# Performance work log

Measured on AMD Instinct MI355X. Metric: run time of the kernel, lower is better.

## Reference

```python
import jax, jax.numpy as jnp
import numpy as np

B, A, D, H, F = 256, 96, 384, 192, 96   # molecules, atoms, feat, hidden, species-MLP out
S = 4                                   # number of species (H, C, N, O)
E = B * A * 32                          # edges (avg degree 32)
CUTOFF = 5.2


def smooth_cutoff(d, cutoff):
    # Smoothstep-style cutoff: 1 at d=0, smoothly -> 0 at d=cutoff (Smoothstep class, reversed edges)
    x = jnp.clip((cutoff - d) / cutoff, 0.0, 1.0)
    return x ** 3 * (x * (6.0 * x - 15.0) + 10.0)


def setup_inputs() -> dict:
    key = jax.random.key(0)
    ks = jax.random.split(key, 9)
    species = jax.random.randint(ks[0], (B, A), 0, S, dtype=jnp.int32)
    in_features = jax.random.normal(ks[1], (B, A, D), dtype=jnp.float32)
    atom_index12 = jax.random.randint(ks[2], (2, E), 0, B * A, dtype=jnp.int32)
    distances = jax.random.uniform(ks[3], (E,), jnp.float32, 0.1, CUTOFF)
    total_charges = jnp.zeros((B,), jnp.float32)
    W1 = jax.random.normal(ks[4], (S, D, H), jnp.float32) / np.float32(np.sqrt(D))
    W2 = jax.random.normal(ks[5], (S, H, F), jnp.float32) / np.float32(np.sqrt(H))
    Wn = jax.random.normal(ks[6], (S, F, F), jnp.float32) / np.float32(np.sqrt(F))
    Wf = jax.random.normal(ks[7], (S, 2 * F, 1), jnp.float32) / np.float32(np.sqrt(2 * F))
    return dict(species=species, in_features=in_features, atom_index12=atom_index12,
                distances=distances, total_charges=total_charges,
                W1=W1, W2=W2, Wn=Wn, Wf=Wf,
                decay_prefactor=jnp.asarray(1.0, jnp.float32),
                decay_factor=jnp.asarray(1.0, jnp.float32))


def reference(species, in_features, atom_index12, distances, total_charges,
              W1, W2, Wn, Wf, decay_prefactor, decay_factor):
    b, a, d = in_features.shape
    n = b * a
    sp = species.reshape(-1)                      # [N]
    x = in_features.reshape(n, d)                 # [N, D]

    # per-species main MLP dispatch: internal[i] = MLP_{sp[i]}(x[i])
    internal = jnp.zeros((n, F), x.dtype)
    for s in range(S):
        mask = (sp == s)[:, None]
        h = jax.nn.gelu(x @ W1[s]) @ W2[s]        # [N, F]
        internal = internal + jnp.where(mask, h, jnp.zeros((), x.dtype))

    # per-species neighbor MLP
    nbr = jnp.zeros((n, F), x.dtype)
    for s in range(S):
        mask = (sp == s)[:, None]
        nbr = nbr + jnp.where(mask, internal @ Wn[s], jnp.zeros((), x.dtype))

    # distance-decayed edge messages: merged[i0] += nbr[i1]*w, merged[i1] += nbr[i0]*w
    decay = (decay_prefactor ** 2) * jnp.exp(-(decay_factor ** 2) * distances) \
            * smooth_cutoff(distances, CUTOFF)    # [E]
    i0, i1 = atom_index12[0], atom_index12[1]
    m_to_i0 = nbr[i1] * decay[:, None]            # [E, F]
    m_to_i1 = nbr[i0] * decay[:, None]
    merged = jax.ops.segment_sum(jnp.concatenate([m_to_i0, m_to_i1], axis=0),
                                 jnp.concatenate([i0, i1], axis=0),
                                 num_segments=n)  # [N, F]

    feats = jnp.concatenate([internal, merged], axis=-1)  # [N, 2F]

    # per-species final head -> precharges
    precharges = jnp.zeros((n,), x.dtype)
    for s in range(S):
        mask = (sp == s)
        precharges = precharges + jnp.where(mask, (feats @ Wf[s])[:, 0], jnp.zeros((), x.dtype))
    precharges = precharges.reshape(b, a)

    # total-charge redistribution (uniform factors, no learned redistribution)
    dummy_mask = species != -1
    factors = 1.0 / dummy_mask.sum(-1, keepdims=True).astype(x.dtype)
    charges = precharges + (total_charges - precharges.sum(-1))[:, None] * factors
    charges = jnp.where(dummy_mask, charges, jnp.zeros((), x.dtype))
    return species, charges, precharges
```

## Files before the change

### kernel.cpp

```cpp
#include <hip/hip_runtime.h>
#include <cstdint>
#include <cstddef>

#define NBm 256
#define NAm 96
#define NDm 384
#define NHm 192
#define NFm 96
#define NSm 4
#define NATOMS (NBm*NAm)
#define NEe (NATOMS*32)
#define CUTOFF_ 5.2f
#define PBLK 256
#define EPB (NEe/PBLK)
#define HBLK 96

typedef __attribute__((ext_vector_type(8))) short short8;
typedef __attribute__((ext_vector_type(4))) float float4v;

__device__ __forceinline__ short f2bf(float f){
  union { float f; unsigned u; } v; v.f = f;
  unsigned r = v.u + 0x7FFFu + ((v.u >> 16) & 1u);
  return (short)(r >> 16);
}

__device__ __forceinline__ float gelu_t(float x){
  float u = 0.7978845608028654f * (x + 0.044715f * x*x*x);
  float e = __expf(-2.0f * fabsf(u));
  float t = (1.0f - e) / (1.0f + e);
  t = (u >= 0.f) ? t : -t;
  return 0.5f * x * (1.0f + t);
}

#define W1N (NSm*NDm*NHm)
#define W2N (NSm*NHm*NFm)
#define WNN (NSm*NFm*NFm)
#define WTOT (W1N+W2N+WNN)
#define WBLK (WTOT/256)
__global__ __launch_bounds__(256) void k_prep(
    const float* __restrict__ W1, const float* __restrict__ W2,
    const float* __restrict__ Wn, const int* __restrict__ sp,
    short* __restrict__ W1t, short* __restrict__ W2t, short* __restrict__ Wnt,
    int* __restrict__ Pcnt){
  int b = blockIdx.x;
  if (b < WBLK){
    int idx = b*256 + threadIdx.x;
    if (idx < W1N){
      int s = idx / (NDm*NHm); int rem = idx - s*NDm*NHm;
      int k = rem / NHm, c = rem - k*NHm;
      W1t[(s*NHm + c)*NDm + k] = f2bf(W1[idx]);
    } else if (idx < W1N + W2N){
      int j = idx - W1N;
      int s = j / (NHm*NFm); int rem = j - s*NHm*NFm;
      int k = rem / NFm, c = rem - k*NFm;
      W2t[(s*NFm + c)*NHm + k] = f2bf(W2[j]);
    } else {
      int j = idx - W1N - W2N;
      int s = j / (NFm*NFm); int rem = j - s*NFm*NFm;
      int k = rem / NFm, c = rem - k*NFm;
      Wnt[(s*NFm + c)*NFm + k] = f2bf(Wn[j]);
    }
  } else {
    __shared__ int h[NSm];
    int t = threadIdx.x;
    if (t < NSm) h[t] = 0;
    __syncthreads();
    int i = (b - WBLK)*256 + t;
    atomicAdd(&h[sp[i]], 1);
    __syncthreads();
    if (t < NSm) Pcnt[(b - WBLK)*NSm + t] = h[t];
  }
}

__global__ __launch_bounds__(256) void k_order(const int* __restrict__ sp,
    const int* __restrict__ Pcnt, int* __restrict__ sps, int* __restrict__ order){
  __shared__ int P[HBLK][NSm];
  __shared__ int stot[NSm], spre[NSm], sscan[NSm+1];
  __shared__ int base[NSm], h[NSm];
  int t = threadIdx.x, b = blockIdx.x;
  if (t < HBLK){
    #pragma unroll
    for (int j=0;j<NSm;j++) P[t][j] = Pcnt[t*NSm + j];
  }
  if (t < NSm) h[t] = 0;
  __syncthreads();
  if (t < NSm){
    int tot = 0, pr = 0;
    for (int bb=0; bb<HBLK; bb++){
      if (bb == b) pr = tot;
      tot += P[bb][t];
    }
    stot[t] = tot; spre[t] = pr;
  }
  __syncthreads();
  if (t == 0){
    int r = 0;
    #pragma unroll
    for (int s2=0;s2<NSm;s2++){ sscan[s2] = r; r += stot[s2]; }
    sscan[NSm] = r;
    if (b == 0){
      #pragma unroll
      for (int s2=0;s2<=NSm;s2++) sps[s2] = sscan[s2];
    }
  }
  __syncthreads();
  if (t < NSm) base[t] = sscan[t] + spre[t];
  __syncthreads();
  int i = b*256 + t;
  int s = sp[i];
  int lr = atomicAdd(&h[s], 1);
  order[base[s] + lr] = i;
}

__global__ __launch_bounds__(256) void k_mlp(
    const float* __restrict__ X, const int* __restrict__ order,
    const int* __restrict__ sps,
    const short* __restrict__ W1t, const short* __restrict__ W2t,
    const short* __restrict__ Wnt, const float* __restrict__ Wf,
    float* __restrict__ pre, float* __restrict__ nd4){
  const int s = blockIdx.y;
  const int s0 = sps[s];
  const int cnt = sps[s+1] - s0;
  const int row0 = blockIdx.x * 64;
  if (row0 >= cnt) return;

  __shared__ short Hs[64][200];
  __shared__ short Is[64][104];
  __shared__ short Ws[19968];
  __shared__ int aids[64];

  const int tid = threadIdx.x;
  if (tid < 64){
    int r = row0 + tid;
    aids[tid] = order[s0 + ((r < cnt) ? r : 0)];
  }
  __syncthreads();

  const int wave = tid >> 6, lane = tid & 63;
  const int lrow = lane & 15, quad = lane >> 4;
  const int arow = wave*16 + lrow;
  const float* xrow = X + (size_t)aids[arow]*NDm + quad*8;

  short8 afs[12];
  #pragma unroll
  for (int kb=0; kb<12; kb++){
    const float* p = xrow + kb*32;
    #pragma unroll
    for (int j=0;j<8;j++) afs[kb][j] = f2bf(p[j]);
  }

  const short* W1s = W1t + (size_t)s*NHm*NDm;
  float4v acc[12];
  #pragma unroll
  for (int i=0;i<12;i++){ acc[i][0]=0.f; acc[i][1]=0.f; acc[i][2]=0.f; acc[i][3]=0.f; }
  for (int kc=0; kc<4; kc++){
    __syncthreads();
    for (int e = tid; e < 192*12; e += 256){
      int c = e / 12, u = e - c*12;
      *(short8*)(&Ws[c*104 + u*8]) = *(const short8*)(W1s + c*NDm + kc*96 + u*8);
    }
    __syncthreads();
    #pragma unroll
    for (int kb3=0; kb3<3; kb3++){
      short8 af = afs[kc*3 + kb3];
      #pragma unroll
      for (int ct=0; ct<12; ct++){
        short8 bfb = *(const short8*)(&Ws[(ct*16 + lrow)*104 + kb3*32 + quad*8]);
        acc[ct] = __builtin_amdgcn_mfma_f32_16x16x32_bf16(af, bfb, acc[ct], 0,0,0);
      }
    }
  }
  #pragma unroll
  for (int ct=0; ct<12; ct++){
    #pragma unroll
    for (int r=0;r<4;r++){
      Hs[wave*16 + quad*4 + r][ct*16 + lrow] = f2bf(gelu_t(acc[ct][r]));
    }
  }

  const short* W2s = W2t + (size_t)s*NFm*NHm;
  float4v acc2[6];
  #pragma unroll
  for (int i=0;i<6;i++){ acc2[i][0]=0.f; acc2[i][1]=0.f; acc2[i][2]=0.f; acc2[i][3]=0.f; }
  __syncthreads();
  for (int e = tid; e < 96*24; e += 256){
    int c = e / 24, u = e - c*24;
    *(short8*)(&Ws[c*200 + u*8]) = *(const short8*)(W2s + c*NHm + u*8);
  }
  __syncthreads();
  for (int kb=0; kb<6; kb++){
    short8 af2 = *(const short8*)(&Hs[wave*16 + lrow][kb*32 + quad*8]);
    #pragma unroll
    for (int ct=0; ct<6; ct++){
      short8 bfb = *(const short8*)(&Ws[(ct*16 + lrow)*200 + kb*32 + quad*8]);
      acc2[ct] = __builtin_amdgcn_mfma_f32_16x16x32_bf16(af2, bfb, acc2[ct], 0,0,0);
    }
  }
  #pragma unroll
  for (int ct=0; ct<6; ct++){
    #pragma unroll
    for (int r=0;r<4;r++){
      Is[wave*16 + quad*4 + r][ct*16 + lrow] = f2bf(acc2[ct][r]);
    }
  }

  {
    float pr[4] = {0.f,0.f,0.f,0.f};
    #pragma unroll
    for (int ct=0; ct<6; ct++){
      float wv = Wf[s*2*NFm + ct*16 + lrow];
      #pragma unroll
      for (int r=0;r<4;r++) pr[r] += acc2[ct][r] * wv;
    }
    #pragma unroll
    for (int m=1; m<16; m<<=1){
      #pragma unroll
      for (int r=0;r<4;r++) pr[r] += __shfl_xor(pr[r], m, 64);
    }
    if (lrow == 0){
      #pragma unroll
      for (int r=0;r<4;r++){
        int row = wave*16 + quad*4 + r;
        if (row0 + row < cnt) pre[aids[row]] = pr[r];
      }
    }
  }

  const short* Wns = Wnt + (size_t)s*NFm*NFm;
  float4v acc3[6];
  #pragma unroll
  for (int i=0;i<6;i++){ acc3[i][0]=0.f; acc3[i][1]=0.f; acc3[i][2]=0.f; acc3[i][3]=0.f; }
  __syncthreads();
  for (int e = tid; e < 96*12; e += 256){
    int c = e / 12, u = e - c*12;
    *(short8*)(&Ws[c*104 + u*8]) = *(const short8*)(Wns + c*NFm + u*8);
  }
  __syncthreads();
  for (int kb=0; kb<3; kb++){
    short8 af3 = *(const short8*)(&Is[wave*16 + lrow][kb*32 + quad*8]);
    #pragma unroll
    for (int ct=0; ct<6; ct++){
      short8 bfb = *(const short8*)(&Ws[(ct*16 + lrow)*104 + kb*32 + quad*8]);
      acc3[ct] = __builtin_amdgcn_mfma_f32_16x16x32_bf16(af3, bfb, acc3[ct], 0,0,0);
    }
  }

  {
    float* NL = (float*)Ws;
    __syncthreads();
    #pragma unroll
    for (int ct=0; ct<6; ct++){
      #pragma unroll
      for (int r=0;r<4;r++){
        NL[(wave*16 + quad*4 + r)*97 + ct*16 + lrow] = acc3[ct][r];
      }
    }
    __syncthreads();
    int row = tid >> 2, t2 = tid & 3;
    if (row0 + row < cnt){
      const float* wfp = Wf + t2*2*NFm + NFm;
      const float* nlr = NL + row*97;
      float a4 = 0.f;
      #pragma unroll 8
      for (int j=0;j<NFm;j++) a4 += nlr[j] * wfp[j];
      nd4[(size_t)aids[row]*4 + t2] = a4;
    }
  }
}

__global__ __launch_bounds__(1024) void k_eacc(const int* __restrict__ ai,
    const float* __restrict__ dist, const float* __restrict__ pref,
    const float* __restrict__ fac, const int* __restrict__ sp,
    const float* __restrict__ nd4, float* __restrict__ part){
  __shared__ float acc[NATOMS];
  const int t = threadIdx.x, b = blockIdx.x;
  #pragma unroll
  for (int k=0;k<NATOMS/1024;k++) acc[k*1024 + t] = 0.f;
  __syncthreads();
  const float p = pref[0], fc = fac[0];
  const int base = b*EPB;
  #pragma unroll
  for (int k=0;k<EPB/1024;k++){
    int e = base + k*1024 + t;
    int i0 = ai[e];
    int i1 = ai[NEe + e];
    float d = dist[e];
    int s0 = sp[i0], s1 = sp[i1];
    float4v n1v = *(const float4v*)(nd4 + (size_t)i1*4);
    float4v n0v = *(const float4v*)(nd4 + (size_t)i0*4);
    float x = (CUTOFF_ - d) * (1.0f/CUTOFF_);
    x = fminf(fmaxf(x, 0.f), 1.f);
    float sc = x*x*x*(x*(6.f*x - 15.f) + 10.f);
    float w = p*p * expf(-fc*fc*d) * sc;
    float a1 = (s0 < 2) ? ((s0 == 0) ? n1v[0] : n1v[1]) : ((s0 == 2) ? n1v[2] : n1v[3]);
    float a0 = (s1 < 2) ? ((s1 == 0) ? n0v[0] : n0v[1]) : ((s1 == 2) ? n0v[2] : n0v[3]);
    atomicAdd(&acc[i0], w * a1);
    atomicAdd(&acc[i1], w * a0);
  }
  __syncthreads();
  float* dst = part + (size_t)b*NATOMS;
  for (int k=t; k<NATOMS/4; k+=1024){
    *(float4v*)(dst + k*4) = *(const float4v*)(&acc[k*4]);
  }
}

__global__ __launch_bounds__(128) void k_final(const float* __restrict__ pre,
    const float* __restrict__ part, const int* __restrict__ sp,
    const float* __restrict__ tc, float* __restrict__ out){
  __shared__ float red[128];
  int mol = blockIdx.x, t = threadIdx.x;
  float pch = 0.f; int s = 0;
  if (t < NAm){
    int a = mol*NAm + t;
    s = sp[a];
    float m = 0.f;
    #pragma unroll 8
    for (int b=0; b<PBLK; b++) m += part[(size_t)b*NATOMS + a];
    pch = pre[a] + m;
  }
  red[t] = (t < NAm) ? pch : 0.f;
  __syncthreads();
  for (int o=64; o>0; o>>=1){
    if (t < o) red[t] += red[t + o];
    __syncthreads();
  }
  float sum = red[0];
  if (t < NAm){
    out[mol*NAm + t] = (float)s;
    out[NATOMS + mol*NAm + t] = pch + (tc[mol] - sum) * (1.0f/96.0f);
    out[2*NATOMS + mol*NAm + t] = pch;
  }
}

extern "C" void kernel_launch(void* const* d_in, const int* in_sizes, int n_in,
                              void* d_out, int out_size, void* d_ws, size_t ws_size,
                              hipStream_t stream) {
  const int*   species = (const int*)  d_in[0];
  const float* X       = (const float*)d_in[1];
  const int*   ai      = (const int*)  d_in[2];
  const float* dist    = (const float*)d_in[3];
  const float* tc      = (const float*)d_in[4];
  const float* W1      = (const float*)d_in[5];
  const float* W2      = (const float*)d_in[6];
  const float* Wn      = (const float*)d_in[7];
  const float* Wf      = (const float*)d_in[8];
  const float* pref    = (const float*)d_in[9];
  const float* fac     = (const float*)d_in[10];
  float* out = (float*)d_out;

  char* w = (char*)d_ws;
  auto alloc = [&](size_t bytes)->char*{
    char* p = w; w += (bytes + 255) & ~(size_t)255; return p;
  };
  int*   Pcnt  = (int*)  alloc((size_t)HBLK*NSm*4);
  int*   sps   = (int*)  alloc(64);
  int*   order = (int*)  alloc((size_t)NATOMS*4);
  float* nd4   = (float*)alloc((size_t)NATOMS*4*4);
  float* pre   = (float*)alloc((size_t)NATOMS*4);
  float* part  = (float*)alloc((size_t)PBLK*NATOMS*4);
  short* W1t   = (short*)alloc((size_t)W1N*2);
  short* W2t   = (short*)alloc((size_t)W2N*2);
  short* Wnt   = (short*)alloc((size_t)WNN*2);

  k_prep<<<WBLK + HBLK, 256, 0, stream>>>(W1, W2, Wn, species, W1t, W2t, Wnt, Pcnt);
  k_order<<<HBLK, 256, 0, stream>>>(species, Pcnt, sps, order);
  dim3 g(NATOMS/64, NSm);
  k_mlp<<<g, 256, 0, stream>>>(X, order, sps, W1t, W2t, Wnt, Wf, pre, nd4);
  k_eacc<<<PBLK, 1024, 0, stream>>>(ai, dist, pref, fac, species, nd4, part);
  k_final<<<NBm, 128, 0, stream>>>(pre, part, species, tc, out);
}
```

Before: 169.5 us.

## Split MLP column tiles across twice as many waves per block

Raises k_mlp from 256 to 512 threads, with pairs of waves sharing a 16-row group and each wave computing half of the output column tiles. This halves the per-wave accumulator registers and MFMA chain length, aiming at more latency hiding and more parallel work per block. The precharge dot product moves from a shuffle reduction to a staged float copy in shared memory read by one wave, and the Wn weight load is overlapped with that staging. Each wave still converts and holds the full X row fragment, so global X loads are duplicated across wave pairs, and an extra sync is added.

```diff
diff --git a/kernel.cpp b/kernel.cpp
--- a/kernel.cpp
+++ b/kernel.cpp
@@ -112,7 +112,7 @@
   order[base[s] + lr] = i;
 }
 
-__global__ __launch_bounds__(256) void k_mlp(
+__global__ __launch_bounds__(512) void k_mlp(
     const float* __restrict__ X, const int* __restrict__ order,
     const int* __restrict__ sps,
     const short* __restrict__ W1t, const short* __restrict__ W2t,
@@ -137,8 +137,10 @@
   __syncthreads();
 
   const int wave = tid >> 6, lane = tid & 63;
+  const int rg = wave >> 1;
+  const int cs = wave & 1;
   const int lrow = lane & 15, quad = lane >> 4;
-  const int arow = wave*16 + lrow;
+  const int arow = rg*16 + lrow;
   const float* xrow = X + (size_t)aids[arow]*NDm + quad*8;
 
   short8 afs[12];
@@ -150,12 +152,12 @@
   }
 
   const short* W1s = W1t + (size_t)s*NHm*NDm;
-  float4v acc[12];
-  #pragma unroll
-  for (int i=0;i<12;i++){ acc[i][0]=0.f; acc[i][1]=0.f; acc[i][2]=0.f; acc[i][3]=0.f; }
+  float4v acc[6];
+  #pragma unroll
+  for (int i=0;i<6;i++){ acc[i][0]=0.f; acc[i][1]=0.f; acc[i][2]=0.f; acc[i][3]=0.f; }
   for (int kc=0; kc<4; kc++){
     __syncthreads();
-    for (int e = tid; e < 192*12; e += 256){
+    for (int e = tid; e < 192*12; e += 512){
       int c = e / 12, u = e - c*12;
       *(short8*)(&Ws[c*104 + u*8]) = *(const short8*)(W1s + c*NDm + kc*96 + u*8);
     }
@@ -164,98 +166,96 @@
     for (int kb3=0; kb3<3; kb3++){
       short8 af = afs[kc*3 + kb3];
       #pragma unroll
-      for (int ct=0; ct<12; ct++){
-        short8 bfb = *(const short8*)(&Ws[(ct*16 + lrow)*104 + kb3*32 + quad*8]);
+      for (int ct=0; ct<6; ct++){
+        int ctt = cs*6 + ct;
+        short8 bfb = *(const short8*)(&Ws[(ctt*16 + lrow)*104 + kb3*32 + quad*8]);
         acc[ct] = __builtin_amdgcn_mfma_f32_16x16x32_bf16(af, bfb, acc[ct], 0,0,0);
       }
     }
   }
   #pragma unroll
-  for (int ct=0; ct<12; ct++){
+  for (int ct=0; ct<6; ct++){
+    int ctt = cs*6 + ct;
     #pragma unroll
     for (int r=0;r<4;r++){
-      Hs[wave*16 + quad*4 + r][ct*16 + lrow] = f2bf(gelu_t(acc[ct][r]));
+      Hs[rg*16 + quad*4 + r][ctt*16 + lrow] = f2bf(gelu_t(acc[ct][r]));
     }
   }
 
   const short* W2s = W2t + (size_t)s*NFm*NHm;
-  float4v acc2[6];
-  #pragma unroll
-  for (int i=0;i<6;i++){ acc2[i][0]=0.f; acc2[i][1]=0.f; acc2[i][2]=0.f; acc2[i][3]=0.f; }
-  __syncthreads();
-  for (int e = tid; e < 96*24; e += 256){
+  float4v acc2[3];
+  #pragma unroll
+  for (int i=0;i<3;i++){ acc2[i][0]=0.f; acc2[i][1]=0.f; acc2[i][2]=0.f; acc2[i][3]=0.f; }
+  __syncthreads();
+  for (int e = tid; e < 96*24; e += 512){
     int c = e / 24, u = e - c*24;
     *(short8*)(&Ws[c*200 + u*8]) = *(const short8*)(W2s + c*NHm + u*8);
   }
   __syncthreads();
   for (int kb=0; kb<6; kb++){
-    short8 af2 = *(const short8*)(&Hs[wave*16 + lrow][kb*32 + quad*8]);
-    #pragma unroll
-    for (int ct=0; ct<6; ct++){
-      short8 bfb = *(const short8*)(&Ws[(ct*16 + lrow)*200 + kb*32 + quad*8]);
+    short8 af2 = *(const short8*)(&Hs[rg*16 + lrow][kb*32 + quad*8]);
+    #pragma unroll
+    for (int ct=0; ct<3; ct++){
+      int ctt = cs*3 + ct;
+      short8 bfb = *(const short8*)(&Ws[(ctt*16 + lrow)*200 + kb*32 + quad*8]);
       acc2[ct] = __builtin_amdgcn_mfma_f32_16x16x32_bf16(af2, bfb, acc2[ct], 0,0,0);
     }
   }
-  #pragma unroll
-  for (int ct=0; ct<6; ct++){
+
+  float* NL = (float*)Hs;
+  __syncthreads();
+  #pragma unroll
+  for (int ct=0; ct<3; ct++){
+    int ctt = cs*3 + ct;
     #pragma unroll
     for (int r=0;r<4;r++){
-      Is[wave*16 + quad*4 + r][ct*16 + lrow] = f2bf(acc2[ct][r]);
-    }
-  }
-
-  {
-    float pr[4] = {0.f,0.f,0.f,0.f};
-    #pragma unroll
-    for (int ct=0; ct<6; ct++){
-      float wv = Wf[s*2*NFm + ct*16 + lrow];
-      #pragma unroll
-      for (int r=0;r<4;r++) pr[r] += acc2[ct][r] * wv;
-    }
-    #pragma unroll
-    for (int m=1; m<16; m<<=1){
-      #pragma unroll
-      for (int r=0;r<4;r++) pr[r] += __shfl_xor(pr[r], m, 64);
-    }
-    if (lrow == 0){
-      #pragma unroll
-      for (int r=0;r<4;r++){
-        int row = wave*16 + quad*4 + r;
-        if (row0 + row < cnt) pre[aids[row]] = pr[r];
-      }
-    }
-  }
-
+      Is[rg*16 + quad*4 + r][ctt*16 + lrow] = f2bf(acc2[ct][r]);
+      NL[(rg*16 + quad*4 + r)*97 + ctt*16 + lrow] = acc2[ct][r];
+    }
+  }
   const short* Wns = Wnt + (size_t)s*NFm*NFm;
-  float4v acc3[6];
-  #pragma unroll
-  for (int i=0;i<6;i++){ acc3[i][0]=0.f; acc3[i][1]=0.f; acc3[i][2]=0.f; acc3[i][3]=0.f; }
-  __syncthreads();
-  for (int e = tid; e < 96*12; e += 256){
+  for (int e = tid; e < 96*12; e += 512){
     int c = e / 12, u = e - c*12;
     *(short8*)(&Ws[c*104 + u*8]) = *(const short8*)(Wns + c*NFm + u*8);
   }
   __syncthreads();
+
+  if (tid < 64){
+    int row = tid;
+    if (row0 + row < cnt){
+      const float* wfp = Wf + s*2*NFm;
+      const float* nlr = NL + row*97;
+      float pr = 0.f;
+      #pragma unroll 8
+      for (int j=0;j<NFm;j++) pr += nlr[j] * wfp[j];
+      pre[aids[row]] = pr;
+    }
+  }
+
+  float4v acc3[3];
+  #pragma unroll
+  for (int i=0;i<3;i++){ acc3[i][0]=0.f; acc3[i][1]=0.f; acc3[i][2]=0.f; acc3[i][3]=0.f; }
   for (int kb=0; kb<3; kb++){
-    short8 af3 = *(const short8*)(&Is[wave*16 + lrow][kb*32 + quad*8]);
-    #pragma unroll
-    for (int ct=0; ct<6; ct++){
-      short8 bfb = *(const short8*)(&Ws[(ct*16 + lrow)*104 + kb*32 + quad*8]);
+    short8 af3 = *(const short8*)(&Is[rg*16 + lrow][kb*32 + quad*8]);
+    #pragma unroll
+    for (int ct=0; ct<3; ct++){
+      int ctt = cs*3 + ct;
+      short8 bfb = *(const short8*)(&Ws[(ctt*16 + lrow)*104 + kb*32 + quad*8]);
       acc3[ct] = __builtin_amdgcn_mfma_f32_16x16x32_bf16(af3, bfb, acc3[ct], 0,0,0);
     }
   }
 
-  {
-    float* NL = (float*)Ws;
-    __syncthreads();
-    #pragma unroll
-    for (int ct=0; ct<6; ct++){
-      #pragma unroll
-      for (int r=0;r<4;r++){
-        NL[(wave*16 + quad*4 + r)*97 + ct*16 + lrow] = acc3[ct][r];
-      }
-    }
-    __syncthreads();
+  __syncthreads();
+  #pragma unroll
+  for (int ct=0; ct<3; ct++){
+    int ctt = cs*3 + ct;
+    #pragma unroll
+    for (int r=0;r<4;r++){
+      NL[(rg*16 + quad*4 + r)*97 + ctt*16 + lrow] = acc3[ct][r];
+    }
+  }
+  __syncthreads();
+  if (tid < 256){
     int row = tid >> 2, t2 = tid & 3;
     if (row0 + row < cnt){
       const float* wfp = Wf + t2*2*NFm + NFm;
@@ -365,7 +365,7 @@
   k_prep<<<WBLK + HBLK, 256, 0, stream>>>(W1, W2, Wn, species, W1t, W2t, Wnt, Pcnt);
   k_order<<<HBLK, 256, 0, stream>>>(species, Pcnt, sps, order);
   dim3 g(NATOMS/64, NSm);
-  k_mlp<<<g, 256, 0, stream>>>(X, order, sps, W1t, W2t, Wnt, Wf, pre, nd4);
+  k_mlp<<<g, 512, 0, stream>>>(X, order, sps, W1t, W2t, Wnt, Wf, pre, nd4);
   k_eacc<<<PBLK, 1024, 0, stream>>>(ai, dist, pref, fac, species, nd4, part);
   k_final<<<NBm, 128, 0, stream>>>(pre, part, species, tc, out);
 }
```

After: 185.4 us. 9.4% more time.

## Prefetch next weight chunk into registers while MFMAs run on current LDS tile

Applied to the files above, without the earlier changes.

The weight staging in k_mlp becomes register double-buffered. Each chunk of W1, W2 and Wn is loaded from global memory into registers before the compute on the previous chunk, then written to shared memory after the barrier. This hides global-load latency behind MFMA work instead of stalling on load-then-sync. In exchange it holds nine extra short8 registers per thread, which could lower occupancy or cause spills.

```diff
diff --git a/kernel.cpp b/kernel.cpp
--- a/kernel.cpp
+++ b/kernel.cpp
@@ -130,6 +130,17 @@
   __shared__ int aids[64];
 
   const int tid = threadIdx.x;
+  const short* W1s = W1t + (size_t)s*NHm*NDm;
+  const short* W2s = W2t + (size_t)s*NFm*NHm;
+  const short* Wns = Wnt + (size_t)s*NFm*NFm;
+
+  short8 wreg[9];
+  #pragma unroll
+  for (int i=0;i<9;i++){
+    int e = tid + i*256, c = e/12, u = e - c*12;
+    wreg[i] = *(const short8*)(W1s + c*NDm + u*8);
+  }
+
   if (tid < 64){
     int r = row0 + tid;
     aids[tid] = order[s0 + ((r < cnt) ? r : 0)];
@@ -149,17 +160,30 @@
     for (int j=0;j<8;j++) afs[kb][j] = f2bf(p[j]);
   }
 
-  const short* W1s = W1t + (size_t)s*NHm*NDm;
   float4v acc[12];
   #pragma unroll
   for (int i=0;i<12;i++){ acc[i][0]=0.f; acc[i][1]=0.f; acc[i][2]=0.f; acc[i][3]=0.f; }
   for (int kc=0; kc<4; kc++){
     __syncthreads();
-    for (int e = tid; e < 192*12; e += 256){
-      int c = e / 12, u = e - c*12;
-      *(short8*)(&Ws[c*104 + u*8]) = *(const short8*)(W1s + c*NDm + kc*96 + u*8);
-    }
-    __syncthreads();
+    #pragma unroll
+    for (int i=0;i<9;i++){
+      int e = tid + i*256, c = e/12, u = e - c*12;
+      *(short8*)(&Ws[c*104 + u*8]) = wreg[i];
+    }
+    __syncthreads();
+    if (kc < 3){
+      #pragma unroll
+      for (int i=0;i<9;i++){
+        int e = tid + i*256, c = e/12, u = e - c*12;
+        wreg[i] = *(const short8*)(W1s + c*NDm + (kc+1)*96 + u*8);
+      }
+    } else {
+      #pragma unroll
+      for (int i=0;i<9;i++){
+        int e = tid + i*256, c = e/24, u = e - c*24;
+        wreg[i] = *(const short8*)(W2s + c*NHm + u*8);
+      }
+    }
     #pragma unroll
     for (int kb3=0; kb3<3; kb3++){
       short8 af = afs[kc*3 + kb3];
@@ -178,16 +202,24 @@
     }
   }
 
-  const short* W2s = W2t + (size_t)s*NFm*NHm;
   float4v acc2[6];
   #pragma unroll
   for (int i=0;i<6;i++){ acc2[i][0]=0.f; acc2[i][1]=0.f; acc2[i][2]=0.f; acc2[i][3]=0.f; }
   __syncthreads();
-  for (int e = tid; e < 96*24; e += 256){
-    int c = e / 24, u = e - c*24;
-    *(short8*)(&Ws[c*200 + u*8]) = *(const short8*)(W2s + c*NHm + u*8);
-  }
-  __syncthreads();
+  #pragma unroll
+  for (int i=0;i<9;i++){
+    int e = tid + i*256, c = e/24, u = e - c*24;
+    *(short8*)(&Ws[c*200 + u*8]) = wreg[i];
+  }
+  __syncthreads();
+  #pragma unroll
+  for (int i=0;i<5;i++){
+    int e = tid + i*256;
+    if (e < 96*12){
+      int c = e/12, u = e - c*12;
+      wreg[i] = *(const short8*)(Wns + c*NFm + u*8);
+    }
+  }
   for (int kb=0; kb<6; kb++){
     short8 af2 = *(const short8*)(&Hs[wave*16 + lrow][kb*32 + quad*8]);
     #pragma unroll
@@ -226,14 +258,17 @@
     }
   }
 
-  const short* Wns = Wnt + (size_t)s*NFm*NFm;
   float4v acc3[6];
   #pragma unroll
   for (int i=0;i<6;i++){ acc3[i][0]=0.f; acc3[i][1]=0.f; acc3[i][2]=0.f; acc3[i][3]=0.f; }
   __syncthreads();
-  for (int e = tid; e < 96*12; e += 256){
-    int c = e / 12, u = e - c*12;
-    *(short8*)(&Ws[c*104 + u*8]) = *(const short8*)(Wns + c*NFm + u*8);
+  #pragma unroll
+  for (int i=0;i<5;i++){
+    int e = tid + i*256;
+    if (e < 96*12){
+      int c = e/12, u = e - c*12;
+      *(short8*)(&Ws[c*104 + u*8]) = wreg[i];
+    }
   }
   __syncthreads();
   for (int kb=0; kb<3; kb++){
```

New measurement: 169.4 us. Within noise of the previous version (-0.1%).
